# Performance work log

Hardware: AMD Instinct MI355X
Metric: run time of the kernel (lower is better)

Reference implementation:

```python
import jax, jax.numpy as jnp
import numpy as np

DIM = 256
NUM_HEADS = 8
HEAD_DIM = DIM // NUM_HEADS  # 32
SCALE = HEAD_DIM ** (-0.5)


def _conv1x1(x, w, b):
    # x: [B,C,H,W], w: [O,C,1,1], b: [O]
    return jnp.einsum('bchw,oc->bohw', x, w[:, :, 0, 0]) + b[None, :, None, None]


def _dwconv3x3(x, w, b):
    # depthwise conv, groups=C, padding=1 (SAME)
    y = jax.lax.conv_general_dilated(
        x, w, window_strides=(1, 1), padding='SAME',
        feature_group_count=x.shape[1],
        dimension_numbers=('NCHW', 'OIHW', 'NCHW'))
    return y + b[None, :, None, None]


def setup_inputs() -> dict:
    key = jax.random.key(0)
    ks = jax.random.split(key, 9)
    s = 0.05
    return {
        'x': jax.random.normal(ks[0], (4, DIM, 48, 48), jnp.float32),
        'w_qk': jax.random.normal(ks[1], (2 * DIM, DIM, 1, 1), jnp.float32) * s,
        'b_qk': jax.random.normal(ks[2], (2 * DIM,), jnp.float32) * s,
        'w_v': jax.random.normal(ks[3], (DIM, DIM, 1, 1), jnp.float32) * s,
        'b_v': jax.random.normal(ks[4], (DIM,), jnp.float32) * s,
        'w_pe': jax.random.normal(ks[5], (DIM, 1, 3, 3), jnp.float32) * s,
        'b_pe': jax.random.normal(ks[6], (DIM,), jnp.float32) * s,
        'w_proj': jax.random.normal(ks[7], (DIM, DIM, 1, 1), jnp.float32) * s,
        'b_proj': jax.random.normal(ks[8], (DIM,), jnp.float32) * s,
    }


def reference(x, w_qk, b_qk, w_v, b_v, w_pe, b_pe, w_proj, b_proj):
    B, C, H, W = x.shape
    N = H * W
    h, d = NUM_HEADS, HEAD_DIM

    qk = _conv1x1(x, w_qk, b_qk).reshape(B, h, 2 * d, N)
    v4 = _conv1x1(x, w_v, b_v)                # [B,C,H,W]
    pe = _dwconv3x3(v4, w_pe, b_pe)           # [B,C,H,W]
    v = v4.reshape(B, h, d, N)

    q, k = qk[:, :, :d, :], qk[:, :, d:, :]   # [B,h,d,N] each
    attn = jnp.einsum('bhdi,bhdj->bhij', q, k) * SCALE  # [B,h,N,N]
    attn = jax.nn.softmax(attn, axis=-1)
    out = jnp.einsum('bhdj,bhij->bhdi', v, attn)        # [B,h,d,N]
    out = out.reshape(B, C, H, W)

    return _conv1x1(out + pe, w_proj, b_proj)
```

## Files before the change

kernel.cpp:

```cpp
#include <hip/hip_runtime.h>
#include <hip/hip_bf16.h>

#define NPIX 2304
#define HW 48
#define CDIM 256
#define NHEADS 8
#define HD 32
#define SCALE_CONST 0.17677669529663687f
#define LOG2E 1.4426950408889634f

typedef __attribute__((ext_vector_type(8))) short  short8v;
typedef __attribute__((ext_vector_type(4))) short  short4v;
typedef __attribute__((ext_vector_type(4))) float  floatx4;

__device__ inline short f2bf(float f) {
    unsigned u = __builtin_bit_cast(unsigned, f);
    u += 0x7FFFu + ((u >> 16) & 1u);
    return (short)(u >> 16);
}
__device__ inline float bf2f(unsigned short us) {
    return __builtin_bit_cast(float, (unsigned)us << 16);
}
__device__ inline float fexp2(float x) {
    return __builtin_amdgcn_exp2f(x);
}

__global__ __launch_bounds__(256) void prep_kernel(
    const float* __restrict__ x,
    short* __restrict__ XT,
    const float* __restrict__ wqk, const float* __restrict__ wv,
    const float* __restrict__ wp,
    short* __restrict__ wqkb, short* __restrict__ wvb, short* __restrict__ wpb)
{
    const int bx = blockIdx.x;
    const int t = threadIdx.x;
    if (bx >= 576) {
        int tid = (bx - 576) * 256 + t;
        for (int idx = tid; idx < 262144; idx += 16384) {
            if (idx < 131072)       wqkb[idx] = f2bf(wqk[idx]);
            else if (idx < 196608)  wvb[idx - 131072] = f2bf(wv[idx - 131072]);
            else                    wpb[idx - 196608] = f2bf(wp[idx - 196608]);
        }
        return;
    }
    __shared__ float sT[64][65];
    const int nt = bx % 36, ct = (bx / 36) & 3, b = bx / 144;
    const int c0 = ct * 64, n0 = nt * 64;
    const float* sp = x + ((size_t)b * 256 + c0) * NPIX + n0;
    const int cl = t >> 6, n = t & 63;
#pragma unroll
    for (int it = 0; it < 16; ++it) {
        int c = it * 4 + cl;
        sT[n][c] = sp[(size_t)c * NPIX + n];
    }
    __syncthreads();
    const int nr = t >> 2, q = t & 3;
    short out[16];
#pragma unroll
    for (int j = 0; j < 16; ++j) out[j] = f2bf(sT[nr][q * 16 + j]);
    short* dp = XT + ((size_t)b * NPIX + n0 + nr) * 256 + c0 + q * 16;
    *(int4*)dp = *(int4*)out;
    *(int4*)(dp + 8) = *(int4*)(out + 8);
}

#define XROW 528

__device__ inline void stage_xt_tile(const short* __restrict__ src_base,
                                     char* __restrict__ sX, int t)
{
    const short* src = src_base + (size_t)(t >> 3) * 256 + (t & 7) * 32;
    char* dst = sX + (t >> 3) * XROW + (t & 7) * 64;
#pragma unroll
    for (int rr = 0; rr < 2; ++rr) {
        const short* s = src + rr * 32 * 256;
        char* d = dst + rr * 32 * XROW;
        *(int4*)d        = *(const int4*)s;
        *(int4*)(d + 16) = *(const int4*)(s + 8);
        *(int4*)(d + 32) = *(const int4*)(s + 16);
        *(int4*)(d + 48) = *(const int4*)(s + 24);
    }
}

__global__ __launch_bounds__(256) void conv_qkv_mfma(
    const short* __restrict__ Wqk,
    const short* __restrict__ Wv,
    const float* __restrict__ bqk,
    const float* __restrict__ bv,
    const short* __restrict__ XT,
    short* __restrict__ QT,
    short* __restrict__ KT,
    short* __restrict__ VB)
{
    __shared__ __align__(16) char sX[64 * XROW];
    const int n0 = blockIdx.x * 64;
    const int b  = blockIdx.z;
    const int t = threadIdx.x, lane = t & 63, w = t >> 6;
    const int l15 = lane & 15, quad = lane >> 4;

    stage_xt_tile(XT + ((size_t)b * NPIX + n0) * 256, sX, t);
    __syncthreads();

    floatx4 accs[2][4];
#pragma unroll
    for (int g = 0; g < 2; ++g) {
        const int og = blockIdx.y + g * 6;
        const bool isV = (og >= 8);
        const short* Wb = isV ? Wv + (size_t)((og - 8) * 64 + w * 16 + l15) * CDIM
                              : Wqk + (size_t)(og * 64 + w * 16 + l15) * CDIM;
#pragma unroll
        for (int ib = 0; ib < 4; ++ib) accs[g][ib] = (floatx4){0.f, 0.f, 0.f, 0.f};
#pragma unroll
        for (int s = 0; s < 8; ++s) {
            short8v af = *(const short8v*)(Wb + s * 32 + quad * 8);
#pragma unroll
            for (int ib = 0; ib < 4; ++ib) {
                short8v bf = *(const short8v*)(sX + (ib * 16 + l15) * XROW + s * 64 + quad * 16);
                accs[g][ib] = __builtin_amdgcn_mfma_f32_16x16x32_bf16(af, bf, accs[g][ib], 0, 0, 0);
            }
        }
    }

#pragma unroll
    for (int g = 0; g < 2; ++g) {
        const int og = blockIdx.y + g * 6;
        const bool isV = (og >= 8);
        __syncthreads();
        if (!isV) {
            const bool isQ = (w < 2);
            const float scl = isQ ? SCALE_CONST * LOG2E : 1.0f;
            float bvv[4];
#pragma unroll
            for (int r = 0; r < 4; ++r) bvv[r] = bqk[og * 64 + w * 16 + quad * 4 + r];
#pragma unroll
            for (int ib = 0; ib < 4; ++ib) {
                short pb[4];
#pragma unroll
                for (int r = 0; r < 4; ++r) pb[r] = f2bf((accs[g][ib][r] + bvv[r]) * scl);
                *(short4v*)(sX + (ib * 16 + l15) * 136 + (w * 16 + quad * 4) * 2) = *(short4v*)pb;
            }
            __syncthreads();
            const int n = t >> 2, q = t & 3;
            int4 v0 = *(const int4*)(sX + n * 136 + q * 32);
            int4 v1 = *(const int4*)(sX + n * 136 + q * 32 + 16);
            short* dst = ((q < 2) ? QT : KT)
                       + ((size_t)(b * 8 + og) * NPIX + n0 + n) * HD + (q & 1) * 16;
            *(int4*)dst = v0;
            *(int4*)(dst + 8) = v1;
        } else {
            const int o0 = (og - 8) * 64 + w * 16 + quad * 4;
            float bvv[4];
#pragma unroll
            for (int r = 0; r < 4; ++r) bvv[r] = bv[o0 + r];
#pragma unroll
            for (int ib = 0; ib < 4; ++ib) {
                short pb[4];
#pragma unroll
                for (int r = 0; r < 4; ++r) pb[r] = f2bf(accs[g][ib][r] + bvv[r]);
                *(short4v*)(sX + (ib * 16 + l15) * 132 + (w * 16 + quad * 4) * 2) = *(short4v*)pb;
            }
            __syncthreads();
            const int o = t >> 2, q = t & 3;
            short tmp[16];
#pragma unroll
            for (int k = 0; k < 16; ++k)
                tmp[k] = *(const short*)(sX + (q * 16 + k) * 132 + o * 2);
            short* dst = VB + ((size_t)b * 256 + (og - 8) * 64 + o) * NPIX + n0 + q * 16;
            *(int4*)dst = *(int4*)tmp;
            *(int4*)(dst + 8) = *(int4*)(tmp + 8);
        }
    }
}

#define KROW 72
#define VROW 136
#define PROW 136
#define SK0 0
#define SK1 4608
#define SV0 9216
#define SV1 13568
#define SP0 17920
#define FL_SMEM 26624
#define DROW 170

__global__ __launch_bounds__(256) void flash_attn_mfma(
    const short* __restrict__ QT,
    const short* __restrict__ KT,
    const short* __restrict__ VB,
    const float* __restrict__ w_pe,
    const float* __restrict__ b_pe,
    short* __restrict__ ST)
{
    __shared__ __align__(16) char smem[FL_SMEM];

    const int hh   = blockIdx.x & 7;
    const int slot = blockIdx.x >> 3;
    const int b    = slot / 36;
    const int i0   = (slot % 36) * 64;
    const int bh   = b * 8 + hh;

    const short* KTp = KT + (size_t)bh * NPIX * HD;
    const short* Vp  = VB + (size_t)(b * 256 + hh * HD) * NPIX;

    const int t    = threadIdx.x;
    const int lane = t & 63;
    const int w    = t >> 6;
    const int l15  = lane & 15;
    const int quad = lane >> 4;

    const short8v qfrag = *(const short8v*)(
        QT + ((size_t)bh * NPIX + i0 + w * 16 + l15) * HD + quad * 8);

    short8v ones;
#pragma unroll
    for (int k = 0; k < 8; ++k) ones[k] = (short)0x3F80;

    char* const sPw = smem + SP0 + w * (16 * PROW);

    floatx4 oacc[2], lacc;
    oacc[0] = (floatx4){0.f, 0.f, 0.f, 0.f};
    oacc[1] = (floatx4){0.f, 0.f, 0.f, 0.f};
    lacc    = (floatx4){0.f, 0.f, 0.f, 0.f};

    const short* ksrc = KTp + (size_t)(t >> 2) * HD + (t & 3) * 8;
    const short* vsrc = Vp + (size_t)(t >> 3) * NPIX + (t & 7) * 8;
    const int koff = (t >> 2) * KROW + (t & 3) * 16;
    const int voff = (t >> 3) * VROW + (t & 7) * 16;

    int4 kst = *(const int4*)ksrc;
    int4 vst = *(const int4*)vsrc;

    for (int it = 0; it < 36; ++it) {
        char* bufK = smem + ((it & 1) ? SK1 : SK0);
        char* bufV = smem + ((it & 1) ? SV1 : SV0);
        *(int2*)(bufK + koff)     = *(int2*)&kst;
        *(int2*)(bufK + koff + 8) = *((int2*)&kst + 1);
        *(int2*)(bufV + voff)     = *(int2*)&vst;
        *(int2*)(bufV + voff + 8) = *((int2*)&vst + 1);
        if (it + 1 < 36) {
            kst = *(const int4*)(ksrc + (size_t)(it + 1) * 64 * HD);
            vst = *(const int4*)(vsrc + (it + 1) * 64);
        }
        __syncthreads();

        floatx4 sacc[4];
#pragma unroll
        for (int jb = 0; jb < 4; ++jb) {
            const char* ka = bufK + (jb * 16 + l15) * KROW + quad * 16;
            short8v af;
            ((int2*)&af)[0] = *(const int2*)ka;
            ((int2*)&af)[1] = *(const int2*)(ka + 8);
            sacc[jb] = __builtin_amdgcn_mfma_f32_16x16x32_bf16(
                af, qfrag, (floatx4){0.f, 0.f, 0.f, 0.f}, 0, 0, 0);
        }

#pragma unroll
        for (int jb = 0; jb < 4; ++jb) {
            unsigned tb[4];
#pragma unroll
            for (int r = 0; r < 4; ++r)
                tb[r] = __builtin_bit_cast(unsigned, fexp2(sacc[jb][r]));
            int2 pw;
            pw.x = (int)__builtin_amdgcn_perm(tb[1], tb[0], 0x07060302u);
            pw.y = (int)__builtin_amdgcn_perm(tb[3], tb[2], 0x07060302u);
            *(int2*)(sPw + l15 * PROW + jb * 32 + quad * 8) = pw;
        }

#pragma unroll
        for (int ks = 0; ks < 2; ++ks) {
            const char* pa = sPw + l15 * PROW + ks * 64 + quad * 16;
            short8v pf;
            ((int2*)&pf)[0] = *(const int2*)pa;
            ((int2*)&pf)[1] = *(const int2*)(pa + 8);
#pragma unroll
            for (int db = 0; db < 2; ++db) {
                const char* va = bufV + (db * 16 + l15) * VROW + ks * 64 + quad * 16;
                short8v vf;
                ((int2*)&vf)[0] = *(const int2*)va;
                ((int2*)&vf)[1] = *(const int2*)(va + 8);
                oacc[db] = __builtin_amdgcn_mfma_f32_16x16x32_bf16(vf, pf, oacc[db], 0, 0, 0);
            }
            lacc = __builtin_amdgcn_mfma_f32_16x16x32_bf16(ones, pf, lacc, 0, 0, 0);
        }
    }

    const float invl = 1.0f / lacc[0];
    __syncthreads();

    short* const sO    = (short*)smem;
    short* const sHalo = (short*)(smem + 4608);

    {
        const int il = w * 16 + l15;
#pragma unroll
        for (int db = 0; db < 2; ++db) {
            short ob[4];
#pragma unroll
            for (int r = 0; r < 4; ++r) ob[r] = f2bf(oacc[db][r] * invl);
            *(short4v*)(sO + il * 36 + db * 16 + quad * 4) = *(short4v*)ob;
        }
    }
    for (int ch8 = t; ch8 < 672; ch8 += 256) {
        int ch = ch8 / 21, off = (ch8 % 21) * 8;
        int base = i0 - 52 + off;
        const short* src = VB + ((size_t)b * 256 + hh * HD + ch) * NPIX;
        short tmp[8];
        if (base >= 0 && base + 8 <= NPIX) {
            *(int4*)tmp = *(const int4*)(src + base);
        } else {
#pragma unroll
            for (int u = 0; u < 8; ++u) {
                int p = base + u;
                tmp[u] = (p >= 0 && p < NPIX) ? src[p] : (short)0;
            }
        }
        *(int4*)&sHalo[ch * DROW + off] = *(int4*)tmp;
    }
    __syncthreads();

    {
        const int d  = t & 31;
        const int pg = t >> 5;
        const int c  = hh * HD + d;
        float wv[9];
#pragma unroll
        for (int k = 0; k < 9; ++k) wv[k] = w_pe[c * 9 + k];
        const float bb = b_pe[c];
        const int px0  = i0 + pg * 8;
        const int col0 = px0 % HW;
        const short* sprow = &sHalo[d * DROW + 52 + pg * 8];
        short* stp = ST + ((size_t)b * NPIX + px0) * 256 + c;

#pragma unroll
        for (int u = 0; u < 8; ++u) {
            int colu = col0 + u; if (colu >= HW) colu -= HW;
            const bool okL = (colu != 0), okR = (colu != HW - 1);
            float a = bb;
#pragma unroll
            for (int dy = 0; dy < 3; ++dy) {
                int ci = u + (dy - 1) * HW;
                a += wv[dy * 3 + 1] * bf2f((unsigned short)sprow[ci]);
                if (okL) a += wv[dy * 3 + 0] * bf2f((unsigned short)sprow[ci - 1]);
                if (okR) a += wv[dy * 3 + 2] * bf2f((unsigned short)sprow[ci + 1]);
            }
            float o = bf2f((unsigned short)sO[(pg * 8 + u) * 36 + d]);
            stp[(size_t)u * 256] = f2bf(o + a);
        }
    }
}

__global__ __launch_bounds__(256) void conv_proj_mfma(
    const short* __restrict__ Wb,
    const float* __restrict__ bias,
    const short* __restrict__ ST,
    float* __restrict__ out)
{
    __shared__ __align__(16) char sX[64 * XROW];
    const int n0 = blockIdx.x * 64;
    const int og = blockIdx.y;
    const int b  = blockIdx.z;
    const int t = threadIdx.x, lane = t & 63, w = t >> 6;
    const int l15 = lane & 15, quad = lane >> 4;

    stage_xt_tile(ST + ((size_t)b * NPIX + n0) * 256, sX, t);
    __syncthreads();

    const short* Arow = Wb + (size_t)(og * 64 + w * 16 + l15) * CDIM;
    floatx4 acc[4];
#pragma unroll
    for (int ib = 0; ib < 4; ++ib) acc[ib] = (floatx4){0.f, 0.f, 0.f, 0.f};
#pragma unroll
    for (int s = 0; s < 8; ++s) {
        short8v af = *(const short8v*)(Arow + s * 32 + quad * 8);
#pragma unroll
        for (int ib = 0; ib < 4; ++ib) {
            short8v bf = *(const short8v*)(sX + (ib * 16 + l15) * XROW + s * 64 + quad * 16);
            acc[ib] = __builtin_amdgcn_mfma_f32_16x16x32_bf16(af, bf, acc[ib], 0, 0, 0);
        }
    }
    __syncthreads();

    {
        float bvv[4];
#pragma unroll
        for (int r = 0; r < 4; ++r) bvv[r] = bias[og * 64 + w * 16 + quad * 4 + r];
        float* sRep = (float*)sX;
#pragma unroll
        for (int r = 0; r < 4; ++r)
#pragma unroll
            for (int ib = 0; ib < 4; ++ib)
                sRep[(w * 16 + quad * 4 + r) * 68 + ib * 16 + l15] = acc[ib][r] + bvv[r];
    }
    __syncthreads();

    const int o = t >> 2, q = t & 3;
    const float* src = (const float*)sX + o * 68 + q * 16;
    float* dst = out + ((size_t)b * 256 + og * 64 + o) * NPIX + n0 + q * 16;
#pragma unroll
    for (int k = 0; k < 4; ++k)
        *(int4*)(dst + k * 4) = *(const int4*)(src + k * 4);
}

extern "C" void kernel_launch(void* const* d_in, const int* in_sizes, int n_in,
                              void* d_out, int out_size, void* d_ws, size_t ws_size,
                              hipStream_t stream) {
    const float* x      = (const float*)d_in[0];
    const float* w_qk   = (const float*)d_in[1];
    const float* b_qk   = (const float*)d_in[2];
    const float* w_v    = (const float*)d_in[3];
    const float* b_v    = (const float*)d_in[4];
    const float* w_pe   = (const float*)d_in[5];
    const float* b_pe   = (const float*)d_in[6];
    const float* w_proj = (const float*)d_in[7];
    const float* b_proj = (const float*)d_in[8];
    float* out = (float*)d_out;

    char* wsb = (char*)d_ws;
    short* ws_xt  = (short*)wsb;  wsb += (size_t)4 * NPIX * 256 * 2;
    short* ws_qt  = (short*)wsb;  wsb += (size_t)32 * NPIX * HD * 2;
    short* ws_kt  = (short*)wsb;  wsb += (size_t)32 * NPIX * HD * 2;
    short* ws_vb  = (short*)wsb;  wsb += (size_t)4 * 256 * NPIX * 2;
    short* ws_st  = (short*)wsb;  wsb += (size_t)4 * NPIX * 256 * 2;
    short* ws_wqk = (short*)wsb;  wsb += (size_t)512 * 256 * 2;
    short* ws_wv  = (short*)wsb;  wsb += (size_t)256 * 256 * 2;
    short* ws_wp  = (short*)wsb;  wsb += (size_t)256 * 256 * 2;

    prep_kernel<<<dim3(640), 256, 0, stream>>>(x, ws_xt, w_qk, w_v, w_proj,
                                               ws_wqk, ws_wv, ws_wp);
    conv_qkv_mfma<<<dim3(36, 6, 4), 256, 0, stream>>>(ws_wqk, ws_wv, b_qk, b_v,
                                                      ws_xt, ws_qt, ws_kt, ws_vb);
    flash_attn_mfma<<<dim3(1152), 256, 0, stream>>>(ws_qt, ws_kt, ws_vb,
                                                    w_pe, b_pe, ws_st);
    conv_proj_mfma<<<dim3(36, 4, 4), 256, 0, stream>>>(ws_wp, b_proj, ws_st, out);
}
```

Baseline: 158.9 us.

## Process two 64-query tiles per attention block to reuse K/V staging

```diff
diff --git a/kernel.cpp b/kernel.cpp
--- a/kernel.cpp
+++ b/kernel.cpp
@@ -179,8 +179,8 @@
 #define SV0 9216
 #define SV1 13568
 #define SP0 17920
-#define FL_SMEM 26624
-#define DROW 170
+#define FL_SMEM 35328
+#define DROW2 248
 
 __global__ __launch_bounds__(256) void flash_attn_mfma(
     const short* __restrict__ QT,
@@ -194,8 +194,8 @@
 
     const int hh   = blockIdx.x & 7;
     const int slot = blockIdx.x >> 3;
-    const int b    = slot / 36;
-    const int i0   = (slot % 36) * 64;
+    const int b    = slot / 18;
+    const int i0A  = (slot % 18) * 128;
     const int bh   = b * 8 + hh;
 
     const short* KTp = KT + (size_t)bh * NPIX * HD;
@@ -207,19 +207,23 @@
     const int l15  = lane & 15;
     const int quad = lane >> 4;
 
-    const short8v qfrag = *(const short8v*)(
-        QT + ((size_t)bh * NPIX + i0 + w * 16 + l15) * HD + quad * 8);
+    const short8v qfragA = *(const short8v*)(
+        QT + ((size_t)bh * NPIX + i0A + w * 16 + l15) * HD + quad * 8);
+    const short8v qfragB = *(const short8v*)(
+        QT + ((size_t)bh * NPIX + i0A + 64 + w * 16 + l15) * HD + quad * 8);
 
     short8v ones;
 #pragma unroll
     for (int k = 0; k < 8; ++k) ones[k] = (short)0x3F80;
 
-    char* const sPw = smem + SP0 + w * (16 * PROW);
-
-    floatx4 oacc[2], lacc;
-    oacc[0] = (floatx4){0.f, 0.f, 0.f, 0.f};
-    oacc[1] = (floatx4){0.f, 0.f, 0.f, 0.f};
-    lacc    = (floatx4){0.f, 0.f, 0.f, 0.f};
+    char* const sPwA = smem + SP0 + w * (16 * PROW);
+    char* const sPwB = smem + SP0 + (4 + w) * (16 * PROW);
+
+    floatx4 oaccA[2], oaccB[2], laccA, laccB;
+    oaccA[0] = (floatx4){0.f, 0.f, 0.f, 0.f};
+    oaccA[1] = (floatx4){0.f, 0.f, 0.f, 0.f};
+    oaccB[0] = oaccA[0]; oaccB[1] = oaccA[0];
+    laccA = oaccA[0]; laccB = oaccA[0];
 
     const short* ksrc = KTp + (size_t)(t >> 2) * HD + (t & 3) * 8;
     const short* vsrc = Vp + (size_t)(t >> 3) * NPIX + (t & 7) * 8;
@@ -242,66 +246,83 @@
         }
         __syncthreads();
 
-        floatx4 sacc[4];
+        floatx4 sA[4], sB[4];
 #pragma unroll
         for (int jb = 0; jb < 4; ++jb) {
             const char* ka = bufK + (jb * 16 + l15) * KROW + quad * 16;
             short8v af;
             ((int2*)&af)[0] = *(const int2*)ka;
             ((int2*)&af)[1] = *(const int2*)(ka + 8);
-            sacc[jb] = __builtin_amdgcn_mfma_f32_16x16x32_bf16(
-                af, qfrag, (floatx4){0.f, 0.f, 0.f, 0.f}, 0, 0, 0);
+            sA[jb] = __builtin_amdgcn_mfma_f32_16x16x32_bf16(
+                af, qfragA, (floatx4){0.f, 0.f, 0.f, 0.f}, 0, 0, 0);
+            sB[jb] = __builtin_amdgcn_mfma_f32_16x16x32_bf16(
+                af, qfragB, (floatx4){0.f, 0.f, 0.f, 0.f}, 0, 0, 0);
         }
 
 #pragma unroll
         for (int jb = 0; jb < 4; ++jb) {
-            unsigned tb[4];
-#pragma unroll
-            for (int r = 0; r < 4; ++r)
-                tb[r] = __builtin_bit_cast(unsigned, fexp2(sacc[jb][r]));
-            int2 pw;
-            pw.x = (int)__builtin_amdgcn_perm(tb[1], tb[0], 0x07060302u);
-            pw.y = (int)__builtin_amdgcn_perm(tb[3], tb[2], 0x07060302u);
-            *(int2*)(sPw + l15 * PROW + jb * 32 + quad * 8) = pw;
+            unsigned ta[4], tb[4];
+#pragma unroll
+            for (int r = 0; r < 4; ++r) {
+                ta[r] = __builtin_bit_cast(unsigned, fexp2(sA[jb][r]));
+                tb[r] = __builtin_bit_cast(unsigned, fexp2(sB[jb][r]));
+            }
+            int2 pwa, pwb;
+            pwa.x = (int)__builtin_amdgcn_perm(ta[1], ta[0], 0x07060302u);
+            pwa.y = (int)__builtin_amdgcn_perm(ta[3], ta[2], 0x07060302u);
+            pwb.x = (int)__builtin_amdgcn_perm(tb[1], tb[0], 0x07060302u);
+            pwb.y = (int)__builtin_amdgcn_perm(tb[3], tb[2], 0x07060302u);
+            *(int2*)(sPwA + l15 * PROW + jb * 32 + quad * 8) = pwa;
+            *(int2*)(sPwB + l15 * PROW + jb * 32 + quad * 8) = pwb;
         }
 
 #pragma unroll
         for (int ks = 0; ks < 2; ++ks) {
-            const char* pa = sPw + l15 * PROW + ks * 64 + quad * 16;
-            short8v pf;
-            ((int2*)&pf)[0] = *(const int2*)pa;
-            ((int2*)&pf)[1] = *(const int2*)(pa + 8);
+            const char* paA = sPwA + l15 * PROW + ks * 64 + quad * 16;
+            const char* paB = sPwB + l15 * PROW + ks * 64 + quad * 16;
+            short8v pfA, pfB;
+            ((int2*)&pfA)[0] = *(const int2*)paA;
+            ((int2*)&pfA)[1] = *(const int2*)(paA + 8);
+            ((int2*)&pfB)[0] = *(const int2*)paB;
+            ((int2*)&pfB)[1] = *(const int2*)(paB + 8);
 #pragma unroll
             for (int db = 0; db < 2; ++db) {
                 const char* va = bufV + (db * 16 + l15) * VROW + ks * 64 + quad * 16;
                 short8v vf;
                 ((int2*)&vf)[0] = *(const int2*)va;
                 ((int2*)&vf)[1] = *(const int2*)(va + 8);
-                oacc[db] = __builtin_amdgcn_mfma_f32_16x16x32_bf16(vf, pf, oacc[db], 0, 0, 0);
-            }
-            lacc = __builtin_amdgcn_mfma_f32_16x16x32_bf16(ones, pf, lacc, 0, 0, 0);
-        }
-    }
-
-    const float invl = 1.0f / lacc[0];
+                oaccA[db] = __builtin_amdgcn_mfma_f32_16x16x32_bf16(vf, pfA, oaccA[db], 0, 0, 0);
+                oaccB[db] = __builtin_amdgcn_mfma_f32_16x16x32_bf16(vf, pfB, oaccB[db], 0, 0, 0);
+            }
+            laccA = __builtin_amdgcn_mfma_f32_16x16x32_bf16(ones, pfA, laccA, 0, 0, 0);
+            laccB = __builtin_amdgcn_mfma_f32_16x16x32_bf16(ones, pfB, laccB, 0, 0, 0);
+        }
+    }
+
+    const float invlA = 1.0f / laccA[0];
+    const float invlB = 1.0f / laccB[0];
     __syncthreads();
 
     short* const sO    = (short*)smem;
-    short* const sHalo = (short*)(smem + 4608);
+    short* const sHalo = (short*)(smem + 9216);
 
     {
         const int il = w * 16 + l15;
 #pragma unroll
         for (int db = 0; db < 2; ++db) {
-            short ob[4];
-#pragma unroll
-            for (int r = 0; r < 4; ++r) ob[r] = f2bf(oacc[db][r] * invl);
-            *(short4v*)(sO + il * 36 + db * 16 + quad * 4) = *(short4v*)ob;
-        }
-    }
-    for (int ch8 = t; ch8 < 672; ch8 += 256) {
-        int ch = ch8 / 21, off = (ch8 % 21) * 8;
-        int base = i0 - 52 + off;
+            short obA[4], obB[4];
+#pragma unroll
+            for (int r = 0; r < 4; ++r) {
+                obA[r] = f2bf(oaccA[db][r] * invlA);
+                obB[r] = f2bf(oaccB[db][r] * invlB);
+            }
+            *(short4v*)(sO + il * 36 + db * 16 + quad * 4) = *(short4v*)obA;
+            *(short4v*)(sO + (64 + il) * 36 + db * 16 + quad * 4) = *(short4v*)obB;
+        }
+    }
+    for (int ch8 = t; ch8 < 928; ch8 += 256) {
+        int ch = ch8 / 29, off = (ch8 % 29) * 8;
+        int base = i0A - 52 + off;
         const short* src = VB + ((size_t)b * 256 + hh * HD + ch) * NPIX;
         short tmp[8];
         if (base >= 0 && base + 8 <= NPIX) {
@@ -313,7 +334,7 @@
                 tmp[u] = (p >= 0 && p < NPIX) ? src[p] : (short)0;
             }
         }
-        *(int4*)&sHalo[ch * DROW + off] = *(int4*)tmp;
+        *(int4*)&sHalo[ch * DROW2 + off] = *(int4*)tmp;
     }
     __syncthreads();
 
@@ -325,25 +346,28 @@
 #pragma unroll
         for (int k = 0; k < 9; ++k) wv[k] = w_pe[c * 9 + k];
         const float bb = b_pe[c];
-        const int px0  = i0 + pg * 8;
-        const int col0 = px0 % HW;
-        const short* sprow = &sHalo[d * DROW + 52 + pg * 8];
-        short* stp = ST + ((size_t)b * NPIX + px0) * 256 + c;
-
-#pragma unroll
-        for (int u = 0; u < 8; ++u) {
-            int colu = col0 + u; if (colu >= HW) colu -= HW;
-            const bool okL = (colu != 0), okR = (colu != HW - 1);
-            float a = bb;
-#pragma unroll
-            for (int dy = 0; dy < 3; ++dy) {
-                int ci = u + (dy - 1) * HW;
-                a += wv[dy * 3 + 1] * bf2f((unsigned short)sprow[ci]);
-                if (okL) a += wv[dy * 3 + 0] * bf2f((unsigned short)sprow[ci - 1]);
-                if (okR) a += wv[dy * 3 + 2] * bf2f((unsigned short)sprow[ci + 1]);
-            }
-            float o = bf2f((unsigned short)sO[(pg * 8 + u) * 36 + d]);
-            stp[(size_t)u * 256] = f2bf(o + a);
+
+#pragma unroll
+        for (int item = 0; item < 2; ++item) {
+            const int px0  = i0A + item * 64 + pg * 8;
+            const int col0 = px0 % HW;
+            const short* sprow = &sHalo[d * DROW2 + 52 + item * 64 + pg * 8];
+            short* stp = ST + ((size_t)b * NPIX + px0) * 256 + c;
+#pragma unroll
+            for (int u = 0; u < 8; ++u) {
+                int colu = col0 + u; if (colu >= HW) colu -= HW;
+                const bool okL = (colu != 0), okR = (colu != HW - 1);
+                float a = bb;
+#pragma unroll
+                for (int dy = 0; dy < 3; ++dy) {
+                    int ci = u + (dy - 1) * HW;
+                    a += wv[dy * 3 + 1] * bf2f((unsigned short)sprow[ci]);
+                    if (okL) a += wv[dy * 3 + 0] * bf2f((unsigned short)sprow[ci - 1]);
+                    if (okR) a += wv[dy * 3 + 2] * bf2f((unsigned short)sprow[ci + 1]);
+                }
+                float o = bf2f((unsigned short)sO[(item * 64 + pg * 8 + u) * 36 + d]);
+                stp[(size_t)u * 256] = f2bf(o + a);
+            }
         }
     }
 }
@@ -428,7 +452,7 @@
                                                ws_wqk, ws_wv, ws_wp);
     conv_qkv_mfma<<<dim3(36, 6, 4), 256, 0, stream>>>(ws_wqk, ws_wv, b_qk, b_v,
                                                       ws_xt, ws_qt, ws_kt, ws_vb);
-    flash_attn_mfma<<<dim3(1152), 256, 0, stream>>>(ws_qt, ws_kt, ws_vb,
-                                                    w_pe, b_pe, ws_st);
+    flash_attn_mfma<<<dim3(576), 256, 0, stream>>>(ws_qt, ws_kt, ws_vb,
+                                                   w_pe, b_pe, ws_st);
     conv_proj_mfma<<<dim3(36, 4, 4), 256, 0, stream>>>(ws_wp, b_proj, ws_st, out);
 }
```

Result: no change. 161.1 us (+1.4%).
